# Optimization experiments

Measured on AMD Instinct MI355X. Metric: run time of the kernel, lower is better.

## Reference

```python
import jax, jax.numpy as jnp
import numpy as np

N_RAYS = 8192
M = 524288
GX, GY, GZ = 160, 160, 128
NFEAT = 12
POS_PE, VIEW_PE = 10, 4
WIDTH = 128
POS_DIM = 3 + 3 * POS_PE * 2      # 63
VIEW_DIM = 3 + 3 * VIEW_PE * 2    # 27
DIM0 = NFEAT + POS_DIM            # 75
ACT_SHIFT = float(np.log(1.0 / (1.0 - 1e-6) - 1.0))  # density bias shift from alpha_init
INTERVAL = 0.5                    # stepsize * voxel_size_ratio
XYZ_MIN, XYZ_MAX = -1.0, 1.0


def posemb(x, n_pe):
    # x: [N,3] -> [N, 3 + 3*n_pe*2], matching cat([x, sin(x*freq), cos(x*freq)])
    freq = 2.0 ** jnp.arange(n_pe, dtype=x.dtype)
    xf = (x[..., None] * freq).reshape(x.shape[0], -1)
    return jnp.concatenate([x, jnp.sin(xf), jnp.cos(xf)], axis=-1)


def trilinear(grid, xyz):
    # grid: [X,Y,Z,C]; xyz: [M,3] in world coords. align_corners=True bilinear (grid_sample).
    sz_f = jnp.array(grid.shape[:3], jnp.float32)
    sz_i = jnp.array(grid.shape[:3], jnp.int32)
    t = (xyz - XYZ_MIN) / (XYZ_MAX - XYZ_MIN) * (sz_f - 1.0)
    t = jnp.clip(t, 0.0, sz_f - 1.0)
    i0 = jnp.clip(jnp.floor(t).astype(jnp.int32), 0, sz_i - 2)
    f = t - i0.astype(t.dtype)
    out = jnp.zeros((xyz.shape[0], grid.shape[-1]), t.dtype)
    for dx in (0, 1):
        for dy in (0, 1):
            for dz in (0, 1):
                w = ((f[:, 0] if dx else 1.0 - f[:, 0])
                     * (f[:, 1] if dy else 1.0 - f[:, 1])
                     * (f[:, 2] if dz else 1.0 - f[:, 2]))
                out = out + w[:, None] * grid[i0[:, 0] + dx, i0[:, 1] + dy, i0[:, 2] + dz]
    return out


def mask_lookup(mask, xyz):
    # nearest-neighbor maskcache_lookup: ijk = round(xyz*scale + shift)
    sz_f = jnp.array(mask.shape, jnp.float32)
    scale = (sz_f - 1.0) / (XYZ_MAX - XYZ_MIN)
    shift = -XYZ_MIN * scale
    ijk = jnp.clip(jnp.round(xyz * scale + shift).astype(jnp.int32), 0,
                   jnp.array(mask.shape, jnp.int32) - 1)
    return mask[ijk[:, 0], ijk[:, 1], ijk[:, 2]]


def alphas2weights(alpha, ray_id, n_rays):
    # segmented T_i = prod_{j<i in ray}(1-alpha_j); weights = T*alpha (ray_id sorted)
    log1a = jnp.log(jnp.clip(1.0 - alpha, 1e-10, 1.0))
    excl = jnp.cumsum(log1a) - log1a                      # global exclusive cumsum
    seg_tot = jax.ops.segment_sum(log1a, ray_id, num_segments=n_rays)
    seg_start = jnp.cumsum(seg_tot) - seg_tot             # exclusive prefix over rays
    T = jnp.exp(excl - seg_start[ray_id])
    weights = T * alpha
    alphainv_last = jnp.exp(seg_tot)
    return weights, alphainv_last


def setup_inputs() -> dict:
    key = jax.random.key(0)
    ks = jax.random.split(key, 16)
    xyz = jax.random.uniform(ks[0], (M, 3), jnp.float32) * (XYZ_MAX - XYZ_MIN) + XYZ_MIN
    ray_id = jnp.sort(jax.random.randint(ks[1], (M,), 0, N_RAYS))
    viewdirs = jax.random.normal(ks[2], (N_RAYS, 3), jnp.float32)
    viewdirs = viewdirs / jnp.linalg.norm(viewdirs, axis=-1, keepdims=True)
    mask = jax.random.uniform(ks[3], (GX, GY, GZ)) > 0.1
    density = jax.random.normal(ks[4], (GX, GY, GZ), jnp.float32) * 0.5
    k0 = jax.random.normal(ks[5], (GX, GY, GZ, NFEAT), jnp.float32) * 0.1
    s = 0.05
    W0 = jax.random.normal(ks[6], (DIM0, WIDTH), jnp.float32) * s
    b0 = jnp.zeros((WIDTH,), jnp.float32)
    W1 = jax.random.normal(ks[7], (WIDTH, WIDTH), jnp.float32) * s
    b1 = jnp.zeros((WIDTH,), jnp.float32)
    W2 = jax.random.normal(ks[8], (WIDTH, WIDTH), jnp.float32) * s
    b2 = jnp.zeros((WIDTH,), jnp.float32)
    Wr = jax.random.normal(ks[9], (WIDTH + VIEW_DIM, 3), jnp.float32) * s
    br = jnp.zeros((3,), jnp.float32)
    return {"xyz": xyz, "ray_id": ray_id, "viewdirs": viewdirs, "mask": mask,
            "density": density, "k0": k0, "W0": W0, "b0": b0, "W1": W1, "b1": b1,
            "W2": W2, "b2": b2, "Wr": Wr, "br": br}


def reference(xyz, ray_id, viewdirs, mask, density, k0, W0, b0, W1, b1, W2, b2, Wr, br):
    # 1) empty-space skipping via mask cache (kept as multiplicative mask for static shapes)
    m = mask_lookup(mask, xyz).astype(xyz.dtype)
    # 2) trilinear density query + raw2alpha
    d = trilinear(density[..., None], xyz)[:, 0]
    alpha = 1.0 - (1.0 + jnp.exp(d + ACT_SHIFT)) ** (-INTERVAL)
    alpha = alpha * m
    # 3) segmented alpha compositing (Alphas2Weights)
    weights, alphainv_last = alphas2weights(alpha, ray_id, N_RAYS)
    # 4) feature query + view MLP -> rgb
    feat = trilinear(k0, xyz)                              # [M, NFEAT]
    h = jnp.concatenate([feat, posemb(xyz, POS_PE)], -1)   # [M, DIM0]
    h = jax.nn.relu(h @ W0 + b0)
    h = jax.nn.relu(h @ W1 + b1)
    h = jax.nn.relu(h @ W2 + b2)
    ve = posemb(viewdirs, VIEW_PE)[ray_id]                 # [M, VIEW_DIM]
    rgb = jax.nn.sigmoid(jnp.concatenate([h, ve], -1) @ Wr + br)
    # 5) composite per ray + white background
    rgb_marched = jax.ops.segment_sum(weights[:, None] * rgb, ray_id, num_segments=N_RAYS)
    rgb_marched = rgb_marched + alphainv_last[:, None] * 1.0
    return rgb_marched
```

## Files before the change

### kernel.cpp

```cpp
#include <hip/hip_runtime.h>
#include <hip/hip_bf16.h>

#define M_SAMPLES 524288
#define NRAYS 8192
#define GXD 160
#define GYD 160
#define GZD 128
#define GYZ (GYD*GZD)
#define NVOX (GXD*GYD*GZD)
#define ACT_SHIFT -13.81550955796f
#define ROWA 136
#define ROWB 136
#define SAMP 64

typedef __bf16 bf16x8 __attribute__((ext_vector_type(8)));
typedef float f32x4 __attribute__((ext_vector_type(4)));
typedef float f32x16 __attribute__((ext_vector_type(16)));
typedef float f32v2 __attribute__((ext_vector_type(2)));

static __device__ inline unsigned short f2bf(float f){
  __hip_bfloat16 h = __float2bfloat16(f);
  unsigned short u; __builtin_memcpy(&u, &h, 2); return u;
}
static __device__ inline float flo(unsigned int u){ return __uint_as_float(u << 16); }
static __device__ inline float fhi(unsigned int u){ return __uint_as_float(u & 0xffff0000u); }

#if defined(__has_builtin)
#if __has_builtin(__builtin_amdgcn_cvt_pk_bf16_f32)
#define HAVE_PK_BF16 1
#endif
#if __has_builtin(__builtin_amdgcn_cvt_pk_f32_fp8) && __has_builtin(__builtin_amdgcn_cvt_pk_fp8_f32)
#define HAVE_FP8 1
#endif
#endif

static __device__ inline unsigned int packbf(float a, float b){
#ifdef HAVE_PK_BF16
  typedef __bf16 bf16v2 __attribute__((ext_vector_type(2)));
  bf16v2 r = __builtin_amdgcn_cvt_pk_bf16_f32(a, b);
  unsigned int u; __builtin_memcpy(&u, &r, 4); return u;
#else
  return (unsigned int)f2bf(a) | ((unsigned int)f2bf(b) << 16);
#endif
}

struct Tri {
  int ix, iy, iz;
  float wx0, wx1, wy0, wy1, wz0, wz1;
};
static __device__ inline Tri tri_setup(float x, float y, float z){
  Tri t;
  float tx = (x+1.f)*0.5f*(float)(GXD-1); tx = fminf(fmaxf(tx,0.f),(float)(GXD-1));
  float ty = (y+1.f)*0.5f*(float)(GYD-1); ty = fminf(fmaxf(ty,0.f),(float)(GYD-1));
  float tz = (z+1.f)*0.5f*(float)(GZD-1); tz = fminf(fmaxf(tz,0.f),(float)(GZD-1));
  t.ix = min((int)tx, GXD-2); t.iy = min((int)ty, GYD-2); t.iz = min((int)tz, GZD-2);
  float fx = tx-t.ix, fy = ty-t.iy, fz = tz-t.iz;
  t.wx0 = 1.f-fx; t.wx1 = fx; t.wy0 = 1.f-fy; t.wy1 = fy; t.wz0 = 1.f-fz; t.wz1 = fz;
  return t;
}

#define NB_REPACK (NVOX/256)
#define NB_W      184
#define NB_RT     (NRAYS/256)
__global__ __launch_bounds__(256) void k_prep(
    const float* __restrict__ density, const float* __restrict__ k0,
    uint4* __restrict__ packed,
    const unsigned int* __restrict__ mw, int* __restrict__ flag,
    const float* __restrict__ W0, const float* __restrict__ W1,
    const float* __restrict__ W2, const float* __restrict__ Wr,
    const float* __restrict__ br,
    unsigned short* __restrict__ wt0, unsigned short* __restrict__ wt1,
    unsigned short* __restrict__ wt2, unsigned short* __restrict__ wtr,
    const float* __restrict__ vd, float* __restrict__ rayterm3)
{
  int b = blockIdx.x;
  if(b < NB_REPACK){
    int v = b*256 + threadIdx.x;
    const float4* kp = (const float4*)(k0 + (size_t)v*12);
    float4 a = kp[0], bb = kp[1], c = kp[2];
#ifdef HAVE_FP8
    uint4 o;
    o.x = __float_as_uint(density[v]);
    int w;
    w = __builtin_amdgcn_cvt_pk_fp8_f32(a.x, a.y, 0, false);
    w = __builtin_amdgcn_cvt_pk_fp8_f32(a.z, a.w, w, true);
    o.y = (unsigned int)w;
    w = __builtin_amdgcn_cvt_pk_fp8_f32(bb.x, bb.y, 0, false);
    w = __builtin_amdgcn_cvt_pk_fp8_f32(bb.z, bb.w, w, true);
    o.z = (unsigned int)w;
    w = __builtin_amdgcn_cvt_pk_fp8_f32(c.x, c.y, 0, false);
    w = __builtin_amdgcn_cvt_pk_fp8_f32(c.z, c.w, w, true);
    o.w = (unsigned int)w;
    packed[v] = o;
#else
    uint4 o0, o1;
    o0.x = __float_as_uint(density[v]);
    o0.y = packbf(a.x, a.y); o0.z = packbf(a.z, a.w); o0.w = packbf(bb.x, bb.y);
    o1.x = packbf(bb.z, bb.w); o1.y = packbf(c.x, c.y); o1.z = packbf(c.z, c.w);
    o1.w = 0;
    packed[(size_t)v*2]   = o0;
    packed[(size_t)v*2+1] = o1;
#endif
    return;
  }
  if(b == NB_REPACK){
    unsigned int v = mw[threadIdx.x & 63];
    unsigned long long any = __ballot(v > 1u);
    if(threadIdx.x == 0) *flag = (any != 0ull) ? 1 : 0;
    return;
  }
  if(b < NB_REPACK + 1 + NB_W){
    int t = (b - NB_REPACK - 1)*256 + threadIdx.x;
    if(t < 128*96){
      int n = t/96, k = t%96;
      wt0[t] = f2bf((k < 75) ? W0[k*128 + n] : 0.f);
    } else if(t < 128*96 + 16384){
      int j = t - 128*96; int n = j/128, k = j%128;
      wt1[j] = f2bf(W1[k*128 + n]);
    } else if(t < 128*96 + 32768){
      int j = t - 128*96 - 16384; int n = j/128, k = j%128;
      wt2[j] = f2bf(W2[k*128 + n]);
    } else if(t < 128*96 + 32768 + 16*128){
      int j = t - 128*96 - 32768; int n = j/128, k = j%128;
      wtr[j] = f2bf((n < 3) ? Wr[k*3 + n] : 0.f);
    }
    return;
  }
  int ray = (b - NB_REPACK - 1 - NB_W)*256 + threadIdx.x;
  if(ray >= NRAYS) return;
  float v0 = vd[ray*3+0], v1 = vd[ray*3+1], v2 = vd[ray*3+2];
  float vej[27];
  vej[0] = v0; vej[1] = v1; vej[2] = v2;
  #pragma unroll
  for(int ci = 0; ci < 3; ++ci){
    float xv = (ci == 0) ? v0 : ((ci == 1) ? v1 : v2);
    #pragma unroll
    for(int p = 0; p < 4; ++p){
      float arg = xv * (float)(1 << p);
      vej[3 + ci*4 + p]  = __sinf(arg);
      vej[15 + ci*4 + p] = __cosf(arg);
    }
  }
  float rt0 = br[0], rt1 = br[1], rt2 = br[2];
  #pragma unroll
  for(int j = 0; j < 27; ++j){
    const float* wr = Wr + (128 + j)*3;
    rt0 += vej[j]*wr[0]; rt1 += vej[j]*wr[1]; rt2 += vej[j]*wr[2];
  }
  rayterm3[ray*3+0] = rt0; rayterm3[ray*3+1] = rt1; rayterm3[ray*3+2] = rt2;
}

template<int KDIM, int SROW>
static __device__ __forceinline__ void mfma_layer(const unsigned short* src,
    const bf16x8* wf, const float* __restrict__ bias, int tile_n,
    f32x16& acc0, f32x16& acc1, int ln, int kh)
{
  constexpr int NS = KDIM/16;
  const unsigned short* abase0 = src + (ln)*SROW + kh*8;
  const unsigned short* abase1 = src + (32 + ln)*SROW + kh*8;
  #pragma unroll
  for(int g = 0; g < 4; ++g){
    float4 bv = *(const float4*)(bias + tile_n*32 + g*8 + kh*4);
    acc0[4*g+0] = bv.x; acc0[4*g+1] = bv.y; acc0[4*g+2] = bv.z; acc0[4*g+3] = bv.w;
  }
  acc1 = acc0;
  __builtin_amdgcn_s_setprio(1);
  #pragma unroll
  for(int st = 0; st < NS; ++st){
    bf16x8 a0 = *(const bf16x8*)(abase0 + st*16);
    bf16x8 a1 = *(const bf16x8*)(abase1 + st*16);
    acc0 = __builtin_amdgcn_mfma_f32_32x32x16_bf16(wf[st], a0, acc0, 0, 0, 0);
    acc1 = __builtin_amdgcn_mfma_f32_32x32x16_bf16(wf[st], a1, acc1, 0, 0, 0);
  }
  __builtin_amdgcn_s_setprio(0);
}

template<int NS>
static __device__ __forceinline__ void load_wf(const unsigned short* wbase, bf16x8* wf){
  #pragma unroll
  for(int st = 0; st < NS; ++st) wf[st] = *(const bf16x8*)(wbase + st*16);
}

template<int DROW>
static __device__ __forceinline__ void epilogue(const f32x16& acc0, const f32x16& acc1,
    unsigned short* dst, int tile_n, int ln, int kh)
{
  #pragma unroll
  for(int rep = 0; rep < 2; ++rep){
    const f32x16& acc = rep ? acc1 : acc0;
    int scol = rep*32 + ln;
    #pragma unroll
    for(int g = 0; g < 4; ++g){
      int n0 = tile_n*32 + g*8 + kh*4;
      unsigned int lo = packbf(fmaxf(acc[4*g+0], 0.f), fmaxf(acc[4*g+1], 0.f));
      unsigned int hi = packbf(fmaxf(acc[4*g+2], 0.f), fmaxf(acc[4*g+3], 0.f));
      unsigned long long o = (unsigned long long)lo | ((unsigned long long)hi << 32);
      *(unsigned long long*)(dst + scol*DROW + n0) = o;
    }
  }
}

template<int PACKED>
__global__ __launch_bounds__(256, 4) void k_mlp(const float* __restrict__ xyz,
    const uint4* __restrict__ packed,
    const float* __restrict__ density, const float* __restrict__ k0,
    const void* __restrict__ mask, const int* __restrict__ flag,
    const int* __restrict__ ray_id,
    const unsigned short* __restrict__ wt0, const unsigned short* __restrict__ wt1,
    const unsigned short* __restrict__ wt2, const unsigned short* __restrict__ wtr,
    const float* __restrict__ b0, const float* __restrict__ b1,
    const float* __restrict__ b2,
    const float* __restrict__ rayterm3, float4* __restrict__ rgba_out)
{
  __shared__ alignas(16) unsigned short hA[SAMP*ROWA];
  __shared__ alignas(16) unsigned short hB[SAMP*ROWB];
  __shared__ float red[SAMP][4];
  __shared__ int ray_s[SAMP];

  int tid = threadIdx.x;
  int lane = tid & 63, wave = tid >> 6;
  int blk = blockIdx.x*SAMP;
  int ln = lane & 31, kh = lane >> 5;

  bf16x8 wf[8];
  load_wf<6>(wt0 + (wave*32 + ln)*96 + kh*8, wf);

  {
    int smp = tid >> 2, corner = tid & 3;
    int i = blk + smp;
    float x = xyz[3*i+0], y = xyz[3*i+1], z = xyz[3*i+2];
    Tri t = tri_setup(x, y, z);
    int dx = corner & 1, dy = corner >> 1;
    float wxy = (dx ? t.wx1 : t.wx0) * (dy ? t.wy1 : t.wy0);
    float w0 = wxy*t.wz0, w1 = wxy*t.wz1;
    size_t vox = (size_t)((t.ix+dx)*GYZ + (t.iy+dy)*GZD + t.iz);
    float pd;
    float pf[12];
#ifdef HAVE_FP8
    if(PACKED){
      uint4 q0 = packed[vox], q1 = packed[vox+1];
      pd = w0*__uint_as_float(q0.x) + w1*__uint_as_float(q1.x);
      f32v2 a, b;
      a = __builtin_amdgcn_cvt_pk_f32_fp8((int)q0.y, false);
      b = __builtin_amdgcn_cvt_pk_f32_fp8((int)q1.y, false);
      pf[0] = w0*a.x + w1*b.x;  pf[1] = w0*a.y + w1*b.y;
      a = __builtin_amdgcn_cvt_pk_f32_fp8((int)q0.y, true);
      b = __builtin_amdgcn_cvt_pk_f32_fp8((int)q1.y, true);
      pf[2] = w0*a.x + w1*b.x;  pf[3] = w0*a.y + w1*b.y;
      a = __builtin_amdgcn_cvt_pk_f32_fp8((int)q0.z, false);
      b = __builtin_amdgcn_cvt_pk_f32_fp8((int)q1.z, false);
      pf[4] = w0*a.x + w1*b.x;  pf[5] = w0*a.y + w1*b.y;
      a = __builtin_amdgcn_cvt_pk_f32_fp8((int)q0.z, true);
      b = __builtin_amdgcn_cvt_pk_f32_fp8((int)q1.z, true);
      pf[6] = w0*a.x + w1*b.x;  pf[7] = w0*a.y + w1*b.y;
      a = __builtin_amdgcn_cvt_pk_f32_fp8((int)q0.w, false);
      b = __builtin_amdgcn_cvt_pk_f32_fp8((int)q1.w, false);
      pf[8] = w0*a.x + w1*b.x;  pf[9] = w0*a.y + w1*b.y;
      a = __builtin_amdgcn_cvt_pk_f32_fp8((int)q0.w, true);
      b = __builtin_amdgcn_cvt_pk_f32_fp8((int)q1.w, true);
      pf[10]= w0*a.x + w1*b.x;  pf[11]= w0*a.y + w1*b.y;
    }
#else
    if(PACKED){
      const uint4* pv = packed + vox*2;
      uint4 q0 = pv[0], q1 = pv[1], q2 = pv[2], q3 = pv[3];
      pd = w0*__uint_as_float(q0.x) + w1*__uint_as_float(q2.x);
      pf[0]  = w0*flo(q0.y) + w1*flo(q2.y);  pf[1]  = w0*fhi(q0.y) + w1*fhi(q2.y);
      pf[2]  = w0*flo(q0.z) + w1*flo(q2.z);  pf[3]  = w0*fhi(q0.z) + w1*fhi(q2.z);
      pf[4]  = w0*flo(q0.w) + w1*flo(q2.w);  pf[5]  = w0*fhi(q0.w) + w1*fhi(q2.w);
      pf[6]  = w0*flo(q1.x) + w1*flo(q3.x);  pf[7]  = w0*fhi(q1.x) + w1*fhi(q3.x);
      pf[8]  = w0*flo(q1.y) + w1*flo(q3.y);  pf[9]  = w0*fhi(q1.y) + w1*fhi(q3.y);
      pf[10] = w0*flo(q1.z) + w1*flo(q3.z);  pf[11] = w0*fhi(q1.z) + w1*fhi(q3.z);
    }
#endif
    if(!PACKED){
      pd = w0*density[vox] + w1*density[vox+1];
      const float4* v = (const float4*)(k0 + vox*12);
      float4 a0 = v[0], a1 = v[1], a2 = v[2];
      float4 c0 = v[3], c1 = v[4], c2 = v[5];
      pf[0] = w0*a0.x + w1*c0.x;  pf[1] = w0*a0.y + w1*c0.y;
      pf[2] = w0*a0.z + w1*c0.z;  pf[3] = w0*a0.w + w1*c0.w;
      pf[4] = w0*a1.x + w1*c1.x;  pf[5] = w0*a1.y + w1*c1.y;
      pf[6] = w0*a1.z + w1*c1.z;  pf[7] = w0*a1.w + w1*c1.w;
      pf[8] = w0*a2.x + w1*c2.x;  pf[9] = w0*a2.y + w1*c2.y;
      pf[10]= w0*a2.z + w1*c2.z;  pf[11]= w0*a2.w + w1*c2.w;
    }
    #pragma unroll
    for(int m2 = 1; m2 < 4; m2 <<= 1){
      pd += __shfl_xor(pd, m2);
      #pragma unroll
      for(int j = 0; j < 12; ++j) pf[j] += __shfl_xor(pf[j], m2);
    }
    if(corner == 0){
      int mx = (int)rintf(x*79.5f + 79.5f); mx = min(max(mx,0), GXD-1);
      int my = (int)rintf(y*79.5f + 79.5f); my = min(max(my,0), GYD-1);
      int mz = (int)rintf(z*63.5f + 63.5f); mz = min(max(mz,0), GZD-1);
      int midx = mx*GYZ + my*GZD + mz;
      bool mm = (*flag) ? (((const unsigned char*)mask)[midx] != 0)
                        : (((const int*)mask)[midx] != 0);
      float e = __expf(pd + ACT_SHIFT);
      float alpha = 1.f - rsqrtf(1.f + e);
      if(!mm) alpha = 0.f;
      red[smp][3] = alpha;
      unsigned int d[8];
      #pragma unroll
      for(int j = 0; j < 6; ++j) d[j] = packbf(pf[2*j], pf[2*j+1]);
      d[6] = packbf(x, y);
      d[7] = packbf(z, __sinf(x));
      uint4* p = (uint4*)(hA + smp*ROWA);
      p[0] = make_uint4(d[0],d[1],d[2],d[3]);
      p[1] = make_uint4(d[4],d[5],d[6],d[7]);
    } else if(corner == 1){
      uint4* p = (uint4*)(hA + smp*ROWA + 80);
      p[0] = make_uint4(0,0,0,0);
      p[1] = make_uint4(0,0,0,0);
      ray_s[smp] = ray_id[i];
    }
  }

  {
    int j = tid >> 6, smp = tid & 63;
    unsigned short* row = hA + smp*ROWA;
    if(j < 3){
      float xv = xyz[3*(blk + smp) + j];
      float s[10], c[10];
      s[0] = __sinf(xv); c[0] = __cosf(xv);
      #pragma unroll
      for(int p = 1; p < 10; ++p){
        float sp = s[p-1], cp = c[p-1];
        s[p] = 2.f*sp*cp;
        c[p] = 1.f - 2.f*sp*sp;
      }
      int sb = 15 + 10*j, cb = 45 + 10*j;
      if(j) row[sb] = f2bf(s[0]);
      #pragma unroll
      for(int p = 0; p < 4; ++p)
        *(unsigned int*)(row + sb + 1 + 2*p) = packbf(s[1+2*p], s[2+2*p]);
      row[sb + 9] = f2bf(s[9]);
      row[cb] = f2bf(c[0]);
      #pragma unroll
      for(int p = 0; p < 4; ++p)
        *(unsigned int*)(row + cb + 1 + 2*p) = packbf(c[1+2*p], c[2+2*p]);
      row[cb + 9] = f2bf(c[9]);
    } else {
      row[75] = 0;
      *(unsigned int*)(row + 76) = 0;
      *(unsigned int*)(row + 78) = 0;
    }
  }
  __syncthreads();

  f32x16 acc0, acc1;

  mfma_layer<96, ROWA>(hA, wf, b0, wave, acc0, acc1, ln, kh);
  load_wf<8>(wt1 + (wave*32 + ln)*128 + kh*8, wf);
  epilogue<ROWB>(acc0, acc1, hB, wave, ln, kh);
  __syncthreads();

  mfma_layer<128, ROWB>(hB, wf, b1, wave, acc0, acc1, ln, kh);
  load_wf<8>(wt2 + (wave*32 + ln)*128 + kh*8, wf);
  epilogue<ROWA>(acc0, acc1, hA, wave, ln, kh);
  __syncthreads();

  int col = lane & 15, q4 = lane >> 4;
  mfma_layer<128, ROWA>(hA, wf, b2, wave, acc0, acc1, ln, kh);
  bf16x8 hw[4];
  {
    const unsigned short* wr = wtr + col*128 + q4*8;
    #pragma unroll
    for(int ks = 0; ks < 4; ++ks) hw[ks] = *(const bf16x8*)(wr + ks*32);
  }
  epilogue<ROWB>(acc0, acc1, hB, wave, ln, kh);
  float rt[4] = {0.f, 0.f, 0.f, 0.f};
  if(col < 3){
    #pragma unroll
    for(int r = 0; r < 4; ++r)
      rt[r] = rayterm3[ray_s[wave*16 + q4*4 + r]*3 + col];
  }
  __syncthreads();

  {
    int mt = wave;
    f32x4 acc = {rt[0], rt[1], rt[2], rt[3]};
    const unsigned short* arow = hB + (mt*16 + col)*ROWB + q4*8;
    __builtin_amdgcn_s_setprio(1);
    #pragma unroll
    for(int ks = 0; ks < 4; ++ks){
      bf16x8 af = *(const bf16x8*)(arow + ks*32);
      acc = __builtin_amdgcn_mfma_f32_16x16x32_bf16(af, hw[ks], acc, 0, 0, 0);
    }
    __builtin_amdgcn_s_setprio(0);
    if(col < 3){
      #pragma unroll
      for(int r = 0; r < 4; ++r){
        int sl = mt*16 + q4*4 + r;
        red[sl][col] = __fdividef(1.f, 1.f + __expf(-acc[r]));
      }
    }
  }
  __syncthreads();

  if(tid < SAMP){
    rgba_out[blk + tid] = make_float4(red[tid][0], red[tid][1], red[tid][2], red[tid][3]);
  }
}

__global__ __launch_bounds__(256) void k_comp2(const int* __restrict__ ray_id,
    const float4* __restrict__ rgba, float* __restrict__ out)
{
  int r = blockIdx.x*4 + (threadIdx.x >> 6);
  int lane = threadIdx.x & 63;
  int lo = 0, hi = M_SAMPLES;
  while(lo < hi){ int mid = (lo+hi) >> 1; if(ray_id[mid] < r) lo = mid+1; else hi = mid; }
  int s = lo;
  int lo2 = s, hi2 = M_SAMPLES;
  while(lo2 < hi2){ int mid = (lo2+hi2) >> 1; if(ray_id[mid] < r+1) lo2 = mid+1; else hi2 = mid; }
  int e = lo2;

  float carry = 1.f;
  float ar = 0.f, ag = 0.f, ab = 0.f;
  for(int base = s; base < e; base += 64){
    int idx = base + lane;
    float4 c = (idx < e) ? rgba[idx] : make_float4(0.f,0.f,0.f,0.f);
    float a = c.w;
    float incl = 1.f - a;
    #pragma unroll
    for(int d2 = 1; d2 < 64; d2 <<= 1){
      float t = __shfl_up(incl, d2);
      if(lane >= d2) incl *= t;
    }
    float excl = __shfl_up(incl, 1);
    if(lane == 0) excl = 1.f;
    float w = carry * excl * a;
    ar += w*c.x; ag += w*c.y; ab += w*c.z;
    carry *= __shfl(incl, 63);
  }
  #pragma unroll
  for(int m2 = 1; m2 < 64; m2 <<= 1){
    ar += __shfl_xor(ar, m2);
    ag += __shfl_xor(ag, m2);
    ab += __shfl_xor(ab, m2);
  }
  if(lane == 0){
    out[3*r+0] = ar + carry;
    out[3*r+1] = ag + carry;
    out[3*r+2] = ab + carry;
  }
}

extern "C" void kernel_launch(void* const* d_in, const int* in_sizes, int n_in,
                              void* d_out, int out_size, void* d_ws, size_t ws_size,
                              hipStream_t stream)
{
  const float* xyz      = (const float*)d_in[0];
  const int*   ray_id   = (const int*)  d_in[1];
  const float* viewdirs = (const float*)d_in[2];
  const void*  mask     =               d_in[3];
  const float* density  = (const float*)d_in[4];
  const float* k0       = (const float*)d_in[5];
  const float* W0 = (const float*)d_in[6];  const float* b0 = (const float*)d_in[7];
  const float* W1 = (const float*)d_in[8];  const float* b1 = (const float*)d_in[9];
  const float* W2 = (const float*)d_in[10]; const float* b2 = (const float*)d_in[11];
  const float* Wr = (const float*)d_in[12]; const float* br = (const float*)d_in[13];
  float* out = (float*)d_out;

  char* ws = (char*)d_ws;
  size_t off = 0;
  auto take = [&](size_t nbytes) -> void* {
    void* p = ws + off;
    off = (off + nbytes + 255) & ~(size_t)255;
    return p;
  };
  int*            flag     = (int*)           take(4);
  unsigned short* wt0      = (unsigned short*)take(128*96*2);
  unsigned short* wt1      = (unsigned short*)take(128*128*2);
  unsigned short* wt2      = (unsigned short*)take(128*128*2);
  unsigned short* wtr      = (unsigned short*)take(16*128*2);
  float*          rayterm3 = (float*)         take((size_t)NRAYS*3*4);
  float4*         rgba_ws  = (float4*)        take((size_t)M_SAMPLES*16);
#ifdef HAVE_FP8
  uint4*          packed   = (uint4*)         take((size_t)NVOX*16);
#else
  uint4*          packed   = (uint4*)         take((size_t)NVOX*32);
#endif
  bool use_packed = (ws_size >= off);

  k_prep<<<NB_REPACK + 1 + NB_W + NB_RT, 256, 0, stream>>>(
      density, k0, packed, (const unsigned int*)mask, flag,
      W0, W1, W2, Wr, br, wt0, wt1, wt2, wtr, viewdirs, rayterm3);
  if(use_packed){
    k_mlp<1><<<M_SAMPLES/SAMP, 256, 0, stream>>>(xyz, packed, density, k0, mask, flag,
                                                 ray_id, wt0, wt1, wt2, wtr,
                                                 b0, b1, b2, rayterm3, rgba_ws);
  } else {
    k_mlp<0><<<M_SAMPLES/SAMP, 256, 0, stream>>>(xyz, packed, density, k0, mask, flag,
                                                 ray_id, wt0, wt1, wt2, wtr,
                                                 b0, b1, b2, rayterm3, rgba_ws);
  }
  k_comp2<<<NRAYS/4, 256, 0, stream>>>(ray_id, rgba_ws, out);
}
```

Baseline: 410.7 us.

## Swizzle LDS activation layout with XOR, hoist mask/ray loads, shuffle fp16-packed features

Replaces the padded 136-element shared-memory rows with a 512-byte-per-row XOR-swizzled layout that packs two samples per row, applied to all MLP layer reads, epilogue writes, and the feature/posenc staging. The mask and ray_id global loads are hoisted ahead of the trilinear gather so their latency overlaps with it. Feature partial sums are packed to fp16 pairs before the cross-lane shuffle reduction, halving the number of shuffles. The fp16 reduction lowers accumulation precision, and the new layout reduces LDS footprint while aiming to avoid bank conflicts.

```diff
diff --git a/kernel.cpp b/kernel.cpp
--- a/kernel.cpp
+++ b/kernel.cpp
@@ -9,14 +9,14 @@
 #define GYZ (GYD*GZD)
 #define NVOX (GXD*GYD*GZD)
 #define ACT_SHIFT -13.81550955796f
-#define ROWA 136
-#define ROWB 136
 #define SAMP 64
+
 
 typedef __bf16 bf16x8 __attribute__((ext_vector_type(8)));
 typedef float f32x4 __attribute__((ext_vector_type(4)));
 typedef float f32x16 __attribute__((ext_vector_type(16)));
 typedef float f32v2 __attribute__((ext_vector_type(2)));
+typedef __fp16 f16x2 __attribute__((ext_vector_type(2)));
 
 static __device__ inline unsigned short f2bf(float f){
   __hip_bfloat16 h = __float2bfloat16(f);
@@ -150,14 +150,15 @@
   rayterm3[ray*3+0] = rt0; rayterm3[ray*3+1] = rt1; rayterm3[ray*3+2] = rt2;
 }
 
-template<int KDIM, int SROW>
+template<int KDIM>
 static __device__ __forceinline__ void mfma_layer(const unsigned short* src,
     const bf16x8* wf, const float* __restrict__ bias, int tile_n,
     f32x16& acc0, f32x16& acc1, int ln, int kh)
 {
   constexpr int NS = KDIM/16;
-  const unsigned short* abase0 = src + (ln)*SROW + kh*8;
-  const unsigned short* abase1 = src + (32 + ln)*SROW + kh*8;
+  const char* s8 = (const char*)src;
+  int lnx = ln << 4;
+  int rowb = ln * 512;
   #pragma unroll
   for(int g = 0; g < 4; ++g){
     float4 bv = *(const float4*)(bias + tile_n*32 + g*8 + kh*4);
@@ -167,8 +168,8 @@
   __builtin_amdgcn_s_setprio(1);
   #pragma unroll
   for(int st = 0; st < NS; ++st){
-    bf16x8 a0 = *(const bf16x8*)(abase0 + st*16);
-    bf16x8 a1 = *(const bf16x8*)(abase1 + st*16);
+    bf16x8 a0 = *(const bf16x8*)(s8 + rowb + ((         (kh<<4) | (st<<5)) ^ lnx));
+    bf16x8 a1 = *(const bf16x8*)(s8 + rowb + (((1<<8) | (kh<<4) | (st<<5)) ^ lnx));
     acc0 = __builtin_amdgcn_mfma_f32_32x32x16_bf16(wf[st], a0, acc0, 0, 0, 0);
     acc1 = __builtin_amdgcn_mfma_f32_32x32x16_bf16(wf[st], a1, acc1, 0, 0, 0);
   }
@@ -181,21 +182,22 @@
   for(int st = 0; st < NS; ++st) wf[st] = *(const bf16x8*)(wbase + st*16);
 }
 
-template<int DROW>
 static __device__ __forceinline__ void epilogue(const f32x16& acc0, const f32x16& acc1,
     unsigned short* dst, int tile_n, int ln, int kh)
 {
+  char* d8 = (char*)dst;
+  int lnx = ln << 4;
+  int rowb = ln * 512;
   #pragma unroll
   for(int rep = 0; rep < 2; ++rep){
     const f32x16& acc = rep ? acc1 : acc0;
-    int scol = rep*32 + ln;
     #pragma unroll
     for(int g = 0; g < 4; ++g){
-      int n0 = tile_n*32 + g*8 + kh*4;
       unsigned int lo = packbf(fmaxf(acc[4*g+0], 0.f), fmaxf(acc[4*g+1], 0.f));
       unsigned int hi = packbf(fmaxf(acc[4*g+2], 0.f), fmaxf(acc[4*g+3], 0.f));
       unsigned long long o = (unsigned long long)lo | ((unsigned long long)hi << 32);
-      *(unsigned long long*)(dst + scol*DROW + n0) = o;
+      int cb = ((rep<<8) | (tile_n<<6) | (g<<4) | (kh<<3)) ^ lnx;
+      *(unsigned long long*)(d8 + rowb + cb) = o;
     }
   }
 }
@@ -212,8 +214,8 @@
     const float* __restrict__ b2,
     const float* __restrict__ rayterm3, float4* __restrict__ rgba_out)
 {
-  __shared__ alignas(16) unsigned short hA[SAMP*ROWA];
-  __shared__ alignas(16) unsigned short hB[SAMP*ROWB];
+  __shared__ alignas(16) unsigned short hA[32*256];
+  __shared__ alignas(16) unsigned short hB[32*256];
   __shared__ float red[SAMP][4];
   __shared__ int ray_s[SAMP];
 
@@ -234,6 +236,16 @@
     float wxy = (dx ? t.wx1 : t.wx0) * (dy ? t.wy1 : t.wy0);
     float w0 = wxy*t.wz0, w1 = wxy*t.wz1;
     size_t vox = (size_t)((t.ix+dx)*GYZ + (t.iy+dy)*GZD + t.iz);
+
+    int mx = (int)rintf(x*79.5f + 79.5f); mx = min(max(mx,0), GXD-1);
+    int my = (int)rintf(y*79.5f + 79.5f); my = min(max(my,0), GYD-1);
+    int mz = (int)rintf(z*63.5f + 63.5f); mz = min(max(mz,0), GZD-1);
+    int midx = mx*GYZ + my*GZD + mz;
+    int flg = *flag;
+    unsigned int mv = flg ? (unsigned int)(((const unsigned char*)mask)[midx])
+                          : ((const unsigned int*)mask)[midx];
+    int rid = ray_id[i];
+
     float pd;
     float pf[12];
 #ifdef HAVE_FP8
@@ -285,42 +297,45 @@
       pf[8] = w0*a2.x + w1*c2.x;  pf[9] = w0*a2.y + w1*c2.y;
       pf[10]= w0*a2.z + w1*c2.z;  pf[11]= w0*a2.w + w1*c2.w;
     }
+
+    f16x2 h[6];
+    #pragma unroll
+    for(int j = 0; j < 6; ++j) h[j] = __builtin_amdgcn_cvt_pkrtz(pf[2*j], pf[2*j+1]);
     #pragma unroll
     for(int m2 = 1; m2 < 4; m2 <<= 1){
       pd += __shfl_xor(pd, m2);
       #pragma unroll
-      for(int j = 0; j < 12; ++j) pf[j] += __shfl_xor(pf[j], m2);
-    }
+      for(int j = 0; j < 6; ++j){
+        int tt = __shfl_xor(__builtin_bit_cast(int, h[j]), m2);
+        h[j] += __builtin_bit_cast(f16x2, tt);
+      }
+    }
+    int R = smp & 31, H = smp >> 5, Rx = R << 4;
+    char* b8 = (char*)hA + R*512;
     if(corner == 0){
-      int mx = (int)rintf(x*79.5f + 79.5f); mx = min(max(mx,0), GXD-1);
-      int my = (int)rintf(y*79.5f + 79.5f); my = min(max(my,0), GYD-1);
-      int mz = (int)rintf(z*63.5f + 63.5f); mz = min(max(mz,0), GZD-1);
-      int midx = mx*GYZ + my*GZD + mz;
-      bool mm = (*flag) ? (((const unsigned char*)mask)[midx] != 0)
-                        : (((const int*)mask)[midx] != 0);
+      bool mm = (mv != 0u);
       float e = __expf(pd + ACT_SHIFT);
       float alpha = 1.f - rsqrtf(1.f + e);
       if(!mm) alpha = 0.f;
       red[smp][3] = alpha;
       unsigned int d[8];
       #pragma unroll
-      for(int j = 0; j < 6; ++j) d[j] = packbf(pf[2*j], pf[2*j+1]);
+      for(int j = 0; j < 6; ++j) d[j] = packbf((float)h[j][0], (float)h[j][1]);
       d[6] = packbf(x, y);
       d[7] = packbf(z, __sinf(x));
-      uint4* p = (uint4*)(hA + smp*ROWA);
-      p[0] = make_uint4(d[0],d[1],d[2],d[3]);
-      p[1] = make_uint4(d[4],d[5],d[6],d[7]);
+      *(uint4*)(b8 + (((H<<8) |  0) ^ Rx)) = make_uint4(d[0],d[1],d[2],d[3]);
+      *(uint4*)(b8 + (((H<<8) | 16) ^ Rx)) = make_uint4(d[4],d[5],d[6],d[7]);
     } else if(corner == 1){
-      uint4* p = (uint4*)(hA + smp*ROWA + 80);
-      p[0] = make_uint4(0,0,0,0);
-      p[1] = make_uint4(0,0,0,0);
-      ray_s[smp] = ray_id[i];
+      *(uint4*)(b8 + (((H<<8) | 160) ^ Rx)) = make_uint4(0,0,0,0);
+      *(uint4*)(b8 + (((H<<8) | 176) ^ Rx)) = make_uint4(0,0,0,0);
+      ray_s[smp] = rid;
     }
   }
 
   {
     int j = tid >> 6, smp = tid & 63;
-    unsigned short* row = hA + smp*ROWA;
+    int R = smp & 31, H8 = (smp >> 5) << 8, Rx = R << 4;
+    char* b8 = (char*)hA + R*512;
     if(j < 3){
       float xv = xyz[3*(blk + smp) + j];
       float s[10], c[10];
@@ -332,45 +347,45 @@
         c[p] = 1.f - 2.f*sp*sp;
       }
       int sb = 15 + 10*j, cb = 45 + 10*j;
-      if(j) row[sb] = f2bf(s[0]);
+      if(j) *(unsigned short*)(b8 + ((H8 | (sb*2)) ^ Rx)) = f2bf(s[0]);
       #pragma unroll
       for(int p = 0; p < 4; ++p)
-        *(unsigned int*)(row + sb + 1 + 2*p) = packbf(s[1+2*p], s[2+2*p]);
-      row[sb + 9] = f2bf(s[9]);
-      row[cb] = f2bf(c[0]);
+        *(unsigned int*)(b8 + ((H8 | ((sb+1+2*p)*2)) ^ Rx)) = packbf(s[1+2*p], s[2+2*p]);
+      *(unsigned short*)(b8 + ((H8 | ((sb+9)*2)) ^ Rx)) = f2bf(s[9]);
+      *(unsigned short*)(b8 + ((H8 | (cb*2)) ^ Rx)) = f2bf(c[0]);
       #pragma unroll
       for(int p = 0; p < 4; ++p)
-        *(unsigned int*)(row + cb + 1 + 2*p) = packbf(c[1+2*p], c[2+2*p]);
-      row[cb + 9] = f2bf(c[9]);
+        *(unsigned int*)(b8 + ((H8 | ((cb+1+2*p)*2)) ^ Rx)) = packbf(c[1+2*p], c[2+2*p]);
+      *(unsigned short*)(b8 + ((H8 | ((cb+9)*2)) ^ Rx)) = f2bf(c[9]);
     } else {
-      row[75] = 0;
-      *(unsigned int*)(row + 76) = 0;
-      *(unsigned int*)(row + 78) = 0;
+      *(unsigned short*)(b8 + ((H8 | 150) ^ Rx)) = 0;
+      *(unsigned int*)  (b8 + ((H8 | 152) ^ Rx)) = 0;
+      *(unsigned int*)  (b8 + ((H8 | 156) ^ Rx)) = 0;
     }
   }
   __syncthreads();
 
   f32x16 acc0, acc1;
 
-  mfma_layer<96, ROWA>(hA, wf, b0, wave, acc0, acc1, ln, kh);
+  mfma_layer<96>(hA, wf, b0, wave, acc0, acc1, ln, kh);
   load_wf<8>(wt1 + (wave*32 + ln)*128 + kh*8, wf);
-  epilogue<ROWB>(acc0, acc1, hB, wave, ln, kh);
+  epilogue(acc0, acc1, hB, wave, ln, kh);
   __syncthreads();
 
-  mfma_layer<128, ROWB>(hB, wf, b1, wave, acc0, acc1, ln, kh);
+  mfma_layer<128>(hB, wf, b1, wave, acc0, acc1, ln, kh);
   load_wf<8>(wt2 + (wave*32 + ln)*128 + kh*8, wf);
-  epilogue<ROWA>(acc0, acc1, hA, wave, ln, kh);
+  epilogue(acc0, acc1, hA, wave, ln, kh);
   __syncthreads();
 
   int col = lane & 15, q4 = lane >> 4;
-  mfma_layer<128, ROWA>(hA, wf, b2, wave, acc0, acc1, ln, kh);
+  mfma_layer<128>(hA, wf, b2, wave, acc0, acc1, ln, kh);
   bf16x8 hw[4];
   {
     const unsigned short* wr = wtr + col*128 + q4*8;
     #pragma unroll
     for(int ks = 0; ks < 4; ++ks) hw[ks] = *(const bf16x8*)(wr + ks*32);
   }
-  epilogue<ROWB>(acc0, acc1, hB, wave, ln, kh);
+  epilogue(acc0, acc1, hB, wave, ln, kh);
   float rt[4] = {0.f, 0.f, 0.f, 0.f};
   if(col < 3){
     #pragma unroll
@@ -381,12 +396,14 @@
 
   {
     int mt = wave;
+    int s = mt*16 + col;
+    int R = s & 31, H = s >> 5, Rx = R << 4;
+    const char* s8 = (const char*)hB + R*512;
     f32x4 acc = {rt[0], rt[1], rt[2], rt[3]};
-    const unsigned short* arow = hB + (mt*16 + col)*ROWB + q4*8;
     __builtin_amdgcn_s_setprio(1);
     #pragma unroll
     for(int ks = 0; ks < 4; ++ks){
-      bf16x8 af = *(const bf16x8*)(arow + ks*32);
+      bf16x8 af = *(const bf16x8*)(s8 + (((H<<8) | (ks<<6) | (q4<<4)) ^ Rx));
       acc = __builtin_amdgcn_mfma_f32_16x16x32_bf16(af, hw[ks], acc, 0, 0, 0);
     }
     __builtin_amdgcn_s_setprio(0);
```

Result: no change. 412.6 us (+0.5%).
